# Kernel tuning notes

Measured on AMD Instinct MI355X. Metric: run time of the kernel, lower is better.

Reference implementation:

```python
import jax, jax.numpy as jnp
import numpy as np

D = 1024   # dim == seq_len L (forced by final proj on [L, L])
N = 16     # SSM state size
K = 3      # conv kernel size, padding=1 -> same length


def setup_inputs() -> dict:
    key = jax.random.key(0)
    ks = jax.random.split(key, 8)
    s = lambda k, shape, sc: (jax.random.normal(k, shape, jnp.float32) * sc)
    return {
        "x": s(ks[0], (2, D, D), 1.0),
        "W_proj": s(ks[1], (D, D), D ** -0.5),
        "b_proj": jnp.zeros((D,), jnp.float32),
        "conv_w": s(ks[2], (D, D, K), (D * K) ** -0.5),  # [out_ch, in_ch, K]
        "conv_b": jnp.zeros((D,), jnp.float32),
        "A_log": jnp.log(jnp.tile(jnp.arange(1, N + 1, dtype=jnp.float32)[None, :], (D, 1))),  # [D, N]
        "W_delta": s(ks[3], (D, D), D ** -0.5),
        "W_B": s(ks[4], (D, N), D ** -0.5),
        "W_C": s(ks[5], (D, N), D ** -0.5),
    }


def _ssm(x, A_log, W_delta, W_B, W_C):
    # Mamba S6 diagonal selective scan. x: [L, D]
    delta = jax.nn.softplus(x @ W_delta)            # [L, D]
    B = x @ W_B                                      # [L, N]
    C = x @ W_C                                      # [L, N]
    A = -jnp.exp(A_log)                              # [D, N]
    Abar = jnp.exp(delta[:, :, None] * A[None])      # [L, D, N]
    Bx = (delta * x)[:, :, None] * B[:, None, :]     # [L, D, N]

    def combine(e1, e2):
        a1, b1 = e1
        a2, b2 = e2
        return a1 * a2, a2 * b1 + b2

    _, h = jax.lax.associative_scan(combine, (Abar, Bx), axis=0)  # h: [L, D, N]
    return jnp.einsum('ldn,ln->ld', h, C)            # [L, D]


def reference(x, W_proj, b_proj, conv_w, conv_b, A_log, W_delta, W_B, W_C):
    p = x @ W_proj.T + b_proj                        # shared proj; [2, L, D]
    xm, xg = p[0], p[1]                              # mirrors `x, x_ = self.proj(x)` unpacking batch==2
    xg = jax.nn.silu(xg)                             # [L, D]
    # Conv1d treats xm as (channels=L, length=D), padding=1 -> same length
    xc = jax.lax.conv_general_dilated(
        xm[None], conv_w, window_strides=(1,), padding=[(1, 1)],
        dimension_numbers=('NCW', 'OIW', 'NCW'))[0] + conv_b[:, None]  # [L, D]
    xc = jax.nn.silu(xc)
    y = _ssm(xc, A_log, W_delta, W_B, W_C)           # [L, D]
    y = y @ xg.T                                     # [L, L]  (x @ x_.transpose(-1,-2))
    return y @ W_proj.T + b_proj                     # final shared proj; [L, L]
```

## Files before the change

kernel.cpp:

```cpp
#include <hip/hip_runtime.h>
#include <math.h>


#define LL 1024
#define DD 1024
#define NS 16
#define CCH 16
#define CLEN 64

typedef short     bf16x8_t __attribute__((ext_vector_type(8)));
typedef float     f32x4_t  __attribute__((ext_vector_type(4)));
typedef unsigned short u16x4_t __attribute__((ext_vector_type(4)));
typedef unsigned short u16x8_t __attribute__((ext_vector_type(8)));

__device__ __forceinline__ float silu_f(float x) { return x / (1.f + expf(-x)); }
__device__ __forceinline__ float softplus_f(float x) {
  return fmaxf(x, 0.f) + log1pf(expf(-fabsf(x)));
}
__device__ __forceinline__ unsigned short f2bf(float f) {
  unsigned int u = __float_as_uint(f);
  u += 0x7fffu + ((u >> 16) & 1u);
  return (unsigned short)(u >> 16);
}

template<int N> __device__ __forceinline__ void s_wait_vmcnt() {
  asm volatile("s_waitcnt vmcnt(%0)" :: "n"(N) : "memory");
}
__device__ __forceinline__ void raw_barrier() {
  asm volatile("s_barrier" ::: "memory");
}

__global__ __launch_bounds__(256) void cast_all(
    const float* __restrict__ x, const float* __restrict__ wp,
    const float* __restrict__ cw, unsigned short* __restrict__ x16,
    unsigned short* __restrict__ wp16, unsigned short* __restrict__ cw16) {
  const size_t i = ((size_t)blockIdx.x * 256 + threadIdx.x) * 4;
  const float* in; unsigned short* out; size_t off;
  if (i < 2097152)      { in = x;  out = x16;  off = 0; }
  else if (i < 3145728) { in = wp; out = wp16; off = 2097152; }
  else                  { in = cw; out = cw16; off = 3145728; }
  const float4 v = *(const float4*)(in + (i - off));
  u16x4_t o; o[0] = f2bf(v.x); o[1] = f2bf(v.y); o[2] = f2bf(v.z); o[3] = f2bf(v.w);
  *(u16x4_t*)(out + (i - off)) = o;
}

__global__ __launch_bounds__(256) void tcastk(const float* __restrict__ W,
                                              unsigned short* __restrict__ out) {
  __shared__ float T[64][65];
  const int t = threadIdx.x;
  const int r = t >> 2, cq = (t & 3) << 4;
  const int d0 = blockIdx.x * 64, k0 = blockIdx.y * 64;
  #pragma unroll
  for (int c = 0; c < 16; c += 4) {
    float4 v = *(const float4*)&W[(size_t)(k0 + r) * DD + d0 + cq + c];
    T[r][cq + c + 0] = v.x; T[r][cq + c + 1] = v.y;
    T[r][cq + c + 2] = v.z; T[r][cq + c + 3] = v.w;
  }
  __syncthreads();
  u16x8_t o0, o1;
  #pragma unroll
  for (int j = 0; j < 8; ++j) o0[j] = f2bf(T[cq + j][r]);
  #pragma unroll
  for (int j = 0; j < 8; ++j) o1[j] = f2bf(T[cq + 8 + j][r]);
  *(u16x8_t*)&out[(size_t)(d0 + r) * DD + k0 + cq] = o0;
  *(u16x8_t*)&out[(size_t)(d0 + r) * DD + k0 + cq + 8] = o1;
}

__global__ __launch_bounds__(256) void bct_cast(const float* __restrict__ WB,
                                                const float* __restrict__ WC,
                                                unsigned short* __restrict__ wcomb) {
  const int b = blockIdx.x;
  const int k = threadIdx.x * 4;
  u16x4_t o;
  if (b < 32) {
    const float* W = (b < 16) ? WB : WC;
    const int n = b & 15;
    #pragma unroll
    for (int j = 0; j < 4; ++j) o[j] = f2bf(W[(size_t)(k + j) * NS + n]);
  } else {
    o[0] = o[1] = o[2] = o[3] = 0;
  }
  *(u16x4_t*)&wcomb[(size_t)(1024 + b) * DD + k] = o;
}

__global__ __launch_bounds__(256) void build_xsht(const unsigned short* __restrict__ xm,
                                                  unsigned short* __restrict__ out) {
  __shared__ unsigned short Xs[64][66];
  const int t = threadIdx.x;
  const int w0 = blockIdx.x * 64, i0 = blockIdx.y * 64;
  {
    const int r = t >> 2, cq = (t & 3) << 4;
    #pragma unroll
    for (int c = 0; c < 16; c += 4) {
      u16x4_t v = *(const u16x4_t*)&xm[(size_t)(i0 + r) * DD + w0 + cq + c];
      Xs[r][1 + cq + c + 0] = v[0]; Xs[r][1 + cq + c + 1] = v[1];
      Xs[r][1 + cq + c + 2] = v[2]; Xs[r][1 + cq + c + 3] = v[3];
    }
  }
  if (t < 64)                 Xs[t][0]       = (w0 > 0)        ? xm[(size_t)(i0 + t) * DD + w0 - 1]  : (unsigned short)0;
  else if (t < 128) { int r = t - 64; Xs[r][65] = (w0 + 64 < DD) ? xm[(size_t)(i0 + r) * DD + w0 + 64] : (unsigned short)0; }
  __syncthreads();
  const int wr = t >> 2, q = t & 3;
  unsigned short vals[48];
  #pragma unroll
  for (int ii = 0; ii < 16; ++ii)
    #pragma unroll
    for (int k = 0; k < 3; ++k)
      vals[ii * 3 + k] = Xs[q * 16 + ii][wr + k];
  #pragma unroll
  for (int s = 0; s < 6; ++s) {
    u16x8_t o;
    #pragma unroll
    for (int j = 0; j < 8; ++j) o[j] = vals[s * 8 + j];
    *(u16x8_t*)&out[(size_t)(w0 + wr) * 3072 + (size_t)i0 * 3 + q * 48 + s * 8] = o;
  }
}

template<int ACT, bool BROW, bool O32, bool O16, bool PART>
__global__ __launch_bounds__(256) void gemm_bf16(
    const unsigned short* __restrict__ A, const unsigned short* __restrict__ B,
    const float* __restrict__ bias, float* __restrict__ C32,
    unsigned short* __restrict__ C16, int M, int N, int K, int Ksl,
    size_t sliceStride)
{
  constexpr int GI = 4;
  __shared__ unsigned short s[3][128 * 64];
  const int tid  = threadIdx.x;
  const int lane = tid & 63;
  const int wv   = tid >> 6;
  const int wm   = wv >> 1, wn = wv & 1;
  const int m0 = blockIdx.y * 64, n0 = blockIdx.x * 64;
  const int wbase = tid & 192;
  const int koff = PART ? blockIdx.z * Ksl : 0;

  f32x4_t acc[2][2];
  #pragma unroll
  for (int i = 0; i < 2; ++i)
    #pragma unroll
    for (int j = 0; j < 2; ++j)
      acc[i][j] = (f32x4_t)(0.f);

  auto stage = [&](int buf, int kbase) {
    #pragma unroll
    for (int it = 0; it < GI; ++it) {
      const int c   = (it << 8) + tid;
      const int r   = c >> 3;
      const int kcg = (c & 7) ^ (r & 7);
      const unsigned short* src = (r < 64)
          ? (A + (size_t)(m0 + r) * K + kbase + kcg * 8)
          : (B + (size_t)(n0 + r - 64) * K + kbase + kcg * 8);
      __builtin_amdgcn_global_load_lds(
          (const __attribute__((address_space(1))) void*)src,
          (__attribute__((address_space(3))) void*)(&s[buf][0] + (size_t)((it << 8) + wbase) * 8),
          16, 0, 0);
    }
  };

  const int NT = Ksl >> 6;
  stage(0, koff);
  stage(1, koff + 64);
  s_wait_vmcnt<GI>();
  raw_barrier();

  for (int t = 0; t < NT; ++t) {
    if (t + 2 < NT) stage((t + 2) % 3, koff + (t + 2) * 64);

    const unsigned short* sb = &s[t % 3][0];
    const int rl = lane & 15, kq = lane >> 4;
    bf16x8_t af[2][2], bfr[2][2];
    #pragma unroll
    for (int mi = 0; mi < 2; ++mi) {
      const int row = wm * 32 + mi * 16 + rl;
      #pragma unroll
      for (int ks = 0; ks < 2; ++ks) {
        const int ch = row * 8 + ((ks * 4 + kq) ^ (row & 7));
        af[mi][ks] = *(const bf16x8_t*)(sb + (size_t)ch * 8);
      }
    }
    #pragma unroll
    for (int ni = 0; ni < 2; ++ni) {
      const int row = 64 + wn * 32 + ni * 16 + rl;
      #pragma unroll
      for (int ks = 0; ks < 2; ++ks) {
        const int ch = row * 8 + ((ks * 4 + kq) ^ (row & 7));
        bfr[ni][ks] = *(const bf16x8_t*)(sb + (size_t)ch * 8);
      }
    }
    #pragma unroll
    for (int mi = 0; mi < 2; ++mi)
      #pragma unroll
      for (int ni = 0; ni < 2; ++ni)
        #pragma unroll
        for (int ks = 0; ks < 2; ++ks)
          acc[mi][ni] = __builtin_amdgcn_mfma_f32_16x16x32_bf16(
              af[mi][ks], bfr[ni][ks], acc[mi][ni], 0, 0, 0);

    if (t + 1 < NT) {
      if (t + 2 < NT) s_wait_vmcnt<GI>();
      else            s_wait_vmcnt<0>();
      raw_barrier();
    }
  }

  const int rl = lane & 15, rg = lane >> 4;
  float* outp = PART ? (C32 + (size_t)blockIdx.z * sliceStride) : C32;
  #pragma unroll
  for (int mi = 0; mi < 2; ++mi) {
    #pragma unroll
    for (int ni = 0; ni < 2; ++ni) {
      const int col = n0 + wn * 32 + ni * 16 + rl;
      #pragma unroll
      for (int j = 0; j < 4; ++j) {
        const int row = m0 + wm * 32 + mi * 16 + rg * 4 + j;
        float v = acc[mi][ni][j];
        if (PART) {
          outp[(size_t)row * N + col] = v;
        } else {
          if (bias) v += BROW ? bias[row] : bias[col];
          if (ACT == 1) v = silu_f(v);
          else if (ACT == 2) v = softplus_f(v);
          else if (ACT == 3) { if (row >= 1024) v = silu_f(v); }
          else if (ACT == 4) { if (row < 1024)  v = softplus_f(v); }
          if (O32) C32[(size_t)row * N + col] = v;
          if (O16) C16[(size_t)row * N + col] = f2bf(v);
        }
      }
    }
  }
}

template<int SK, int ACT, bool O32, bool O16>
__global__ __launch_bounds__(256) void reduce_k(
    const float* __restrict__ part, size_t sliceStride,
    const float* __restrict__ bias,
    float* __restrict__ C32, unsigned short* __restrict__ C16)
{
  const size_t idx = ((size_t)blockIdx.x * 256 + threadIdx.x) * 4;
  const int row = (int)(idx >> 10), col = (int)(idx & 1023);
  float4 s = *(const float4*)&part[idx];
  #pragma unroll
  for (int z = 1; z < SK; ++z) {
    const float4 p = *(const float4*)&part[(size_t)z * sliceStride + idx];
    s.x += p.x; s.y += p.y; s.z += p.z; s.w += p.w;
  }
  float v[4] = {s.x, s.y, s.z, s.w};
  if (bias) {
    const float4 bv = *(const float4*)&bias[col];
    v[0] += bv.x; v[1] += bv.y; v[2] += bv.z; v[3] += bv.w;
  }
  #pragma unroll
  for (int j = 0; j < 4; ++j) {
    if (ACT == 2) v[j] = softplus_f(v[j]);
    else if (ACT == 4) { if (row < 1024) v[j] = softplus_f(v[j]); }
  }
  if (O32) { float4 o; o.x = v[0]; o.y = v[1]; o.z = v[2]; o.w = v[3];
             *(float4*)&C32[idx] = o; }
  if (O16) { u16x4_t o; o[0] = f2bf(v[0]); o[1] = f2bf(v[1]);
             o[2] = f2bf(v[2]); o[3] = f2bf(v[3]);
             *(u16x4_t*)&C16[idx] = o; }
}

template<int SK>
__global__ __launch_bounds__(256) void reduce_conv_t(
    const float* __restrict__ part, const float* __restrict__ cb,
    unsigned short* __restrict__ xc16, float* __restrict__ xcT)
{
  __shared__ float T[64][65];
  const int t = threadIdx.x;
  const int r = t >> 4;
  const int cq = (t & 15) << 2;
  const int r0 = blockIdx.y * 64, c0 = blockIdx.x * 64;
  #pragma unroll
  for (int rr = 0; rr < 64; rr += 16) {
    const int row = r0 + r + rr;
    const size_t base = (size_t)row * 1024 + c0 + cq;
    float4 s = *(const float4*)&part[base];
    #pragma unroll
    for (int z = 1; z < SK; ++z) {
      const float4 p = *(const float4*)&part[(size_t)z * (1024 * 1024) + base];
      s.x += p.x; s.y += p.y; s.z += p.z; s.w += p.w;
    }
    const float b = cb[row];
    float v[4] = {silu_f(s.x + b), silu_f(s.y + b), silu_f(s.z + b), silu_f(s.w + b)};
    u16x4_t o16; o16[0] = f2bf(v[0]); o16[1] = f2bf(v[1]);
    o16[2] = f2bf(v[2]); o16[3] = f2bf(v[3]);
    *(u16x4_t*)&xc16[base] = o16;
    T[r + rr][cq + 0] = v[0]; T[r + rr][cq + 1] = v[1];
    T[r + rr][cq + 2] = v[2]; T[r + rr][cq + 3] = v[3];
  }
  __syncthreads();
  #pragma unroll
  for (int rr = 0; rr < 64; rr += 16) {
    float4 o;
    o.x = T[cq + 0][r + rr]; o.y = T[cq + 1][r + rr];
    o.z = T[cq + 2][r + rr]; o.w = T[cq + 3][r + rr];
    *(float4*)&xcT[(size_t)(c0 + r + rr) * LL + r0 + cq] = o;
  }
}

__global__ __launch_bounds__(256) void scan_p1(
    const float* __restrict__ deltaT, const float* __restrict__ xcT,
    const float* __restrict__ BT, const float* __restrict__ A_log,
    float* __restrict__ P, float* __restrict__ H)
{
  const int tid = threadIdx.x;
  const int n = tid & 15, dl = tid >> 4;
  const int d = blockIdx.y * 16 + dl;
  const int c = blockIdx.x;
  const int l0 = c * CLEN;
  const float Av = -expf(A_log[d * NS + n]);
  float h = 0.f, p = 1.f;
  for (int j = 0; j < CLEN; j += 4) {
    const float4 dv = *(const float4*)&deltaT[(size_t)d * LL + l0 + j];
    const float4 xv = *(const float4*)&xcT[(size_t)d * LL + l0 + j];
    const float4 bv = *(const float4*)&BT[(size_t)n * LL + l0 + j];
    const float dvu[4] = {dv.x, dv.y, dv.z, dv.w};
    const float xvu[4] = {xv.x, xv.y, xv.z, xv.w};
    const float bvu[4] = {bv.x, bv.y, bv.z, bv.w};
    #pragma unroll
    for (int u = 0; u < 4; ++u) {
      const float ab = expf(dvu[u] * Av);
      h = fmaf(ab, h, dvu[u] * xvu[u] * bvu[u]);
      p *= ab;
    }
  }
  const int idx = d * NS + n;
  P[(size_t)c * (DD * NS) + idx] = p;
  H[(size_t)c * (DD * NS) + idx] = h;
}

__global__ __launch_bounds__(256) void scan_p2(const float* __restrict__ P,
                                               const float* __restrict__ H,
                                               float* __restrict__ Hin) {
  const int idx = blockIdx.x * 256 + threadIdx.x;
  float hin = 0.f;
  Hin[idx] = 0.f;
  #pragma unroll
  for (int c = 1; c < CCH; ++c) {
    hin = fmaf(P[(size_t)(c - 1) * (DD * NS) + idx], hin,
               H[(size_t)(c - 1) * (DD * NS) + idx]);
    Hin[(size_t)c * (DD * NS) + idx] = hin;
  }
}

__global__ __launch_bounds__(256) void scan_p3(
    const float* __restrict__ deltaT, const float* __restrict__ xcT,
    const float* __restrict__ BT, const float* __restrict__ CT,
    const float* __restrict__ Hin, const float* __restrict__ A_log,
    unsigned short* __restrict__ y16)
{
  const int tid = threadIdx.x;
  const int n = tid & 15, dl = tid >> 4;
  const int d = blockIdx.y * 16 + dl;
  const int c = blockIdx.x;
  const int l0 = c * CLEN;
  const float Av = -expf(A_log[d * NS + n]);
  float h = Hin[(size_t)c * (DD * NS) + d * NS + n];
  for (int j = 0; j < CLEN; j += 4) {
    const float4 dv = *(const float4*)&deltaT[(size_t)d * LL + l0 + j];
    const float4 xv = *(const float4*)&xcT[(size_t)d * LL + l0 + j];
    const float4 bv = *(const float4*)&BT[(size_t)n * LL + l0 + j];
    const float4 cv = *(const float4*)&CT[(size_t)n * LL + l0 + j];
    const float dvu[4] = {dv.x, dv.y, dv.z, dv.w};
    const float xvu[4] = {xv.x, xv.y, xv.z, xv.w};
    const float bvu[4] = {bv.x, bv.y, bv.z, bv.w};
    const float cvu[4] = {cv.x, cv.y, cv.z, cv.w};
    #pragma unroll
    for (int u = 0; u < 4; ++u) {
      const int l = l0 + j + u;
      const float ab = expf(dvu[u] * Av);
      h = fmaf(ab, h, dvu[u] * xvu[u] * bvu[u]);
      float contrib = h * cvu[u];
      contrib += __shfl_xor(contrib, 1);
      contrib += __shfl_xor(contrib, 2);
      contrib += __shfl_xor(contrib, 4);
      contrib += __shfl_xor(contrib, 8);
      if (n == 0) y16[(size_t)l * DD + d] = f2bf(contrib);
    }
  }
}

extern "C" void kernel_launch(void* const* d_in, const int* in_sizes, int n_in,
                              void* d_out, int out_size, void* d_ws, size_t ws_size,
                              hipStream_t stream) {
  const float* x       = (const float*)d_in[0];
  const float* W_proj  = (const float*)d_in[1];
  const float* b_proj  = (const float*)d_in[2];
  const float* conv_w  = (const float*)d_in[3];
  const float* conv_b  = (const float*)d_in[4];
  const float* A_log   = (const float*)d_in[5];
  const float* W_delta = (const float*)d_in[6];
  const float* W_B     = (const float*)d_in[7];
  const float* W_C     = (const float*)d_in[8];
  float* out = (float*)d_out;

  char* w = (char*)d_ws;
  const size_t QMB = 256 * 1024;
  unsigned short* wp16    = (unsigned short*)(w);
  unsigned short* pbuf    = (unsigned short*)(w + 8  * QMB);
  unsigned short* xm16    = pbuf;
  unsigned short* xg16    = pbuf + 1024 * 1024;
  unsigned short* wcomb16 = (unsigned short*)(w + 24 * QMB);
  unsigned short* xc16    = (unsigned short*)(w + 34 * QMB);
  float*          xcT32   = (float*)(w + 42 * QMB);
  unsigned short* x16     = (unsigned short*)(w + 58 * QMB);
  float*          dcomb32 = (float*)(w + 58 * QMB);
  float*          deltaT32= dcomb32;
  float*          BT32    = dcomb32 + (size_t)1024 * 1024;
  float*          CT32    = dcomb32 + (size_t)1040 * 1024;
  unsigned short* cw16    = (unsigned short*)(w + 75 * QMB);
  unsigned short* y16     = (unsigned short*)(w + 75 * QMB);
  float*          Pc      = (float*)(w + 83 * QMB);
  float*          Hc      = (float*)(w + 87 * QMB);
  float*          HinC    = (float*)(w + 91 * QMB);
  unsigned short* out116  = (unsigned short*)(w + 87 * QMB);
  unsigned short* xsht    = (unsigned short*)(w + 99 * QMB);
  float*          part    = (float*)(w + 123 * QMB);
  (void)ws_size;

  const dim3 blk(256);

  cast_all<<<dim3(6144), blk, 0, stream>>>(x, W_proj, conv_w, x16, wp16, cw16);
  tcastk<<<dim3(16, 16), blk, 0, stream>>>(W_delta, wcomb16);
  bct_cast<<<dim3(128), blk, 0, stream>>>(W_B, W_C, wcomb16);

  gemm_bf16<3, false, false, true, false><<<dim3(16, 32), blk, 0, stream>>>(
      x16, wp16, b_proj, nullptr, pbuf, 2048, 1024, 1024, 1024, 0);
  build_xsht<<<dim3(16, 16), blk, 0, stream>>>(xm16, xsht);
  gemm_bf16<0, false, true, false, true><<<dim3(16, 16, 2), blk, 0, stream>>>(
      cw16, xsht, nullptr, part, nullptr, 1024, 1024, 3072, 1536,
      (size_t)1024 * 1024);
  reduce_conv_t<2><<<dim3(16, 16), blk, 0, stream>>>(part, conv_b, xc16, xcT32);
  gemm_bf16<0, false, true, false, true><<<dim3(16, 18, 2), blk, 0, stream>>>(
      wcomb16, xc16, nullptr, part, nullptr, 1152, 1024, 1024, 512,
      (size_t)1152 * 1024);
  reduce_k<2, 4, true, false><<<dim3(1056), blk, 0, stream>>>(
      part, (size_t)1152 * 1024, nullptr, dcomb32, nullptr);
  scan_p1<<<dim3(CCH, DD / 16), blk, 0, stream>>>(deltaT32, xcT32, BT32, A_log, Pc, Hc);
  scan_p2<<<dim3(64), blk, 0, stream>>>(Pc, Hc, HinC);
  scan_p3<<<dim3(CCH, DD / 16), blk, 0, stream>>>(deltaT32, xcT32, BT32, CT32, HinC, A_log, y16);
  gemm_bf16<0, false, true, false, true><<<dim3(16, 16, 2), blk, 0, stream>>>(
      y16, xg16, nullptr, part, nullptr, 1024, 1024, 1024, 512,
      (size_t)1024 * 1024);
  reduce_k<2, 0, false, true><<<dim3(1024), blk, 0, stream>>>(
      part, (size_t)1024 * 1024, nullptr, nullptr, out116);
  gemm_bf16<0, false, true, false, true><<<dim3(16, 16, 2), blk, 0, stream>>>(
      out116, wp16, nullptr, part, nullptr, 1024, 1024, 1024, 512,
      (size_t)1024 * 1024);
  reduce_k<2, 0, true, false><<<dim3(1024), blk, 0, stream>>>(
      part, (size_t)1024 * 1024, b_proj, out, nullptr);
}
```

Measured before the change: 203.3 us.

## Merge prep casts, drop split-K reductions, fold scan carry into final pass

Fuses the three weight and input cast kernels into one launch. Removes split-K from the delta/B/C, y@xg^T and final projection GEMMs, so each writes its epilogue directly and the reduce_k kernels go away. Also trims the padded row count of the combined weight. The scan's separate carry-propagation kernel is removed, and each chunk recomputes its incoming state serially from the per-chunk products. This cuts launches and partial-sum traffic, at the cost of fewer workgroups per GEMM (256 on a large GPU) and redundant carry work in later chunks.

```diff
diff --git a/kernel.cpp b/kernel.cpp
--- a/kernel.cpp
+++ b/kernel.cpp
@@ -30,57 +30,56 @@
   asm volatile("s_barrier" ::: "memory");
 }
 
-__global__ __launch_bounds__(256) void cast_all(
+__global__ __launch_bounds__(256) void prep_all(
     const float* __restrict__ x, const float* __restrict__ wp,
-    const float* __restrict__ cw, unsigned short* __restrict__ x16,
-    unsigned short* __restrict__ wp16, unsigned short* __restrict__ cw16) {
-  const size_t i = ((size_t)blockIdx.x * 256 + threadIdx.x) * 4;
-  const float* in; unsigned short* out; size_t off;
-  if (i < 2097152)      { in = x;  out = x16;  off = 0; }
-  else if (i < 3145728) { in = wp; out = wp16; off = 2097152; }
-  else                  { in = cw; out = cw16; off = 3145728; }
-  const float4 v = *(const float4*)(in + (i - off));
-  u16x4_t o; o[0] = f2bf(v.x); o[1] = f2bf(v.y); o[2] = f2bf(v.z); o[3] = f2bf(v.w);
-  *(u16x4_t*)(out + (i - off)) = o;
-}
-
-__global__ __launch_bounds__(256) void tcastk(const float* __restrict__ W,
-                                              unsigned short* __restrict__ out) {
-  __shared__ float T[64][65];
+    const float* __restrict__ cw, const float* __restrict__ wd,
+    const float* __restrict__ WB, const float* __restrict__ WC,
+    unsigned short* __restrict__ x16, unsigned short* __restrict__ wp16,
+    unsigned short* __restrict__ cw16, unsigned short* __restrict__ wcomb) {
+  const int b = blockIdx.x;
   const int t = threadIdx.x;
-  const int r = t >> 2, cq = (t & 3) << 4;
-  const int d0 = blockIdx.x * 64, k0 = blockIdx.y * 64;
-  #pragma unroll
-  for (int c = 0; c < 16; c += 4) {
-    float4 v = *(const float4*)&W[(size_t)(k0 + r) * DD + d0 + cq + c];
-    T[r][cq + c + 0] = v.x; T[r][cq + c + 1] = v.y;
-    T[r][cq + c + 2] = v.z; T[r][cq + c + 3] = v.w;
-  }
-  __syncthreads();
-  u16x8_t o0, o1;
-  #pragma unroll
-  for (int j = 0; j < 8; ++j) o0[j] = f2bf(T[cq + j][r]);
-  #pragma unroll
-  for (int j = 0; j < 8; ++j) o1[j] = f2bf(T[cq + 8 + j][r]);
-  *(u16x8_t*)&out[(size_t)(d0 + r) * DD + k0 + cq] = o0;
-  *(u16x8_t*)&out[(size_t)(d0 + r) * DD + k0 + cq + 8] = o1;
-}
-
-__global__ __launch_bounds__(256) void bct_cast(const float* __restrict__ WB,
-                                                const float* __restrict__ WC,
-                                                unsigned short* __restrict__ wcomb) {
-  const int b = blockIdx.x;
-  const int k = threadIdx.x * 4;
-  u16x4_t o;
-  if (b < 32) {
-    const float* W = (b < 16) ? WB : WC;
-    const int n = b & 15;
-    #pragma unroll
-    for (int j = 0; j < 4; ++j) o[j] = f2bf(W[(size_t)(k + j) * NS + n]);
+  if (b < 6144) {
+    const size_t i = ((size_t)b * 256 + t) * 4;
+    const float* in; unsigned short* out; size_t off;
+    if (i < 2097152)      { in = x;  out = x16;  off = 0; }
+    else if (i < 3145728) { in = wp; out = wp16; off = 2097152; }
+    else                  { in = cw; out = cw16; off = 3145728; }
+    const float4 v = *(const float4*)(in + (i - off));
+    u16x4_t o; o[0] = f2bf(v.x); o[1] = f2bf(v.y); o[2] = f2bf(v.z); o[3] = f2bf(v.w);
+    *(u16x4_t*)(out + (i - off)) = o;
+  } else if (b < 6400) {
+    __shared__ float T[64][65];
+    const int bi = b - 6144;
+    const int d0 = (bi & 15) << 6, k0 = (bi >> 4) << 6;
+    const int r = t >> 2, cq = (t & 3) << 4;
+    #pragma unroll
+    for (int c = 0; c < 16; c += 4) {
+      float4 v = *(const float4*)&wd[(size_t)(k0 + r) * DD + d0 + cq + c];
+      T[r][cq + c + 0] = v.x; T[r][cq + c + 1] = v.y;
+      T[r][cq + c + 2] = v.z; T[r][cq + c + 3] = v.w;
+    }
+    __syncthreads();
+    u16x8_t o0, o1;
+    #pragma unroll
+    for (int j = 0; j < 8; ++j) o0[j] = f2bf(T[cq + j][r]);
+    #pragma unroll
+    for (int j = 0; j < 8; ++j) o1[j] = f2bf(T[cq + 8 + j][r]);
+    *(u16x8_t*)&wcomb[(size_t)(d0 + r) * DD + k0 + cq] = o0;
+    *(u16x8_t*)&wcomb[(size_t)(d0 + r) * DD + k0 + cq + 8] = o1;
   } else {
-    o[0] = o[1] = o[2] = o[3] = 0;
-  }
-  *(u16x4_t*)&wcomb[(size_t)(1024 + b) * DD + k] = o;
+    const int bb = b - 6400;
+    const int k = t * 4;
+    u16x4_t o;
+    if (bb < 32) {
+      const float* W = (bb < 16) ? WB : WC;
+      const int n = bb & 15;
+      #pragma unroll
+      for (int j = 0; j < 4; ++j) o[j] = f2bf(W[(size_t)(k + j) * NS + n]);
+    } else {
+      o[0] = o[1] = o[2] = o[3] = 0;
+    }
+    *(u16x4_t*)&wcomb[(size_t)(1024 + bb) * DD + k] = o;
+  }
 }
 
 __global__ __launch_bounds__(256) void build_xsht(const unsigned short* __restrict__ xm,
@@ -229,38 +228,6 @@
   }
 }
 
-template<int SK, int ACT, bool O32, bool O16>
-__global__ __launch_bounds__(256) void reduce_k(
-    const float* __restrict__ part, size_t sliceStride,
-    const float* __restrict__ bias,
-    float* __restrict__ C32, unsigned short* __restrict__ C16)
-{
-  const size_t idx = ((size_t)blockIdx.x * 256 + threadIdx.x) * 4;
-  const int row = (int)(idx >> 10), col = (int)(idx & 1023);
-  float4 s = *(const float4*)&part[idx];
-  #pragma unroll
-  for (int z = 1; z < SK; ++z) {
-    const float4 p = *(const float4*)&part[(size_t)z * sliceStride + idx];
-    s.x += p.x; s.y += p.y; s.z += p.z; s.w += p.w;
-  }
-  float v[4] = {s.x, s.y, s.z, s.w};
-  if (bias) {
-    const float4 bv = *(const float4*)&bias[col];
-    v[0] += bv.x; v[1] += bv.y; v[2] += bv.z; v[3] += bv.w;
-  }
-  #pragma unroll
-  for (int j = 0; j < 4; ++j) {
-    if (ACT == 2) v[j] = softplus_f(v[j]);
-    else if (ACT == 4) { if (row < 1024) v[j] = softplus_f(v[j]); }
-  }
-  if (O32) { float4 o; o.x = v[0]; o.y = v[1]; o.z = v[2]; o.w = v[3];
-             *(float4*)&C32[idx] = o; }
-  if (O16) { u16x4_t o; o[0] = f2bf(v[0]); o[1] = f2bf(v[1]);
-             o[2] = f2bf(v[2]); o[3] = f2bf(v[3]);
-             *(u16x4_t*)&C16[idx] = o; }
-}
-
-template<int SK>
 __global__ __launch_bounds__(256) void reduce_conv_t(
     const float* __restrict__ part, const float* __restrict__ cb,
     unsigned short* __restrict__ xc16, float* __restrict__ xcT)
@@ -275,11 +242,8 @@
     const int row = r0 + r + rr;
     const size_t base = (size_t)row * 1024 + c0 + cq;
     float4 s = *(const float4*)&part[base];
-    #pragma unroll
-    for (int z = 1; z < SK; ++z) {
-      const float4 p = *(const float4*)&part[(size_t)z * (1024 * 1024) + base];
-      s.x += p.x; s.y += p.y; s.z += p.z; s.w += p.w;
-    }
+    const float4 p = *(const float4*)&part[(size_t)(1024 * 1024) + base];
+    s.x += p.x; s.y += p.y; s.z += p.z; s.w += p.w;
     const float b = cb[row];
     float v[4] = {silu_f(s.x + b), silu_f(s.y + b), silu_f(s.z + b), silu_f(s.w + b)};
     u16x4_t o16; o16[0] = f2bf(v[0]); o16[1] = f2bf(v[1]);
@@ -329,33 +293,22 @@
   H[(size_t)c * (DD * NS) + idx] = h;
 }
 
-__global__ __launch_bounds__(256) void scan_p2(const float* __restrict__ P,
-                                               const float* __restrict__ H,
-                                               float* __restrict__ Hin) {
-  const int idx = blockIdx.x * 256 + threadIdx.x;
-  float hin = 0.f;
-  Hin[idx] = 0.f;
-  #pragma unroll
-  for (int c = 1; c < CCH; ++c) {
-    hin = fmaf(P[(size_t)(c - 1) * (DD * NS) + idx], hin,
-               H[(size_t)(c - 1) * (DD * NS) + idx]);
-    Hin[(size_t)c * (DD * NS) + idx] = hin;
-  }
-}
-
-__global__ __launch_bounds__(256) void scan_p3(
+__global__ __launch_bounds__(256) void scan_p3c(
     const float* __restrict__ deltaT, const float* __restrict__ xcT,
     const float* __restrict__ BT, const float* __restrict__ CT,
-    const float* __restrict__ Hin, const float* __restrict__ A_log,
-    unsigned short* __restrict__ y16)
+    const float* __restrict__ P, const float* __restrict__ Hc,
+    const float* __restrict__ A_log, unsigned short* __restrict__ y16)
 {
   const int tid = threadIdx.x;
   const int n = tid & 15, dl = tid >> 4;
   const int d = blockIdx.y * 16 + dl;
   const int c = blockIdx.x;
   const int l0 = c * CLEN;
-  const float Av = -expf(A_log[d * NS + n]);
-  float h = Hin[(size_t)c * (DD * NS) + d * NS + n];
+  const int idx = d * NS + n;
+  const float Av = -expf(A_log[idx]);
+  float h = 0.f;
+  for (int cc = 0; cc < c; ++cc)
+    h = fmaf(P[(size_t)cc * (DD * NS) + idx], h, Hc[(size_t)cc * (DD * NS) + idx]);
   for (int j = 0; j < CLEN; j += 4) {
     const float4 dv = *(const float4*)&deltaT[(size_t)d * LL + l0 + j];
     const float4 xv = *(const float4*)&xcT[(size_t)d * LL + l0 + j];
@@ -412,7 +365,6 @@
   unsigned short* y16     = (unsigned short*)(w + 75 * QMB);
   float*          Pc      = (float*)(w + 83 * QMB);
   float*          Hc      = (float*)(w + 87 * QMB);
-  float*          HinC    = (float*)(w + 91 * QMB);
   unsigned short* out116  = (unsigned short*)(w + 87 * QMB);
   unsigned short* xsht    = (unsigned short*)(w + 99 * QMB);
   float*          part    = (float*)(w + 123 * QMB);
@@ -420,33 +372,22 @@
 
   const dim3 blk(256);
 
-  cast_all<<<dim3(6144), blk, 0, stream>>>(x, W_proj, conv_w, x16, wp16, cw16);
-  tcastk<<<dim3(16, 16), blk, 0, stream>>>(W_delta, wcomb16);
-  bct_cast<<<dim3(128), blk, 0, stream>>>(W_B, W_C, wcomb16);
-
+  prep_all<<<dim3(6528), blk, 0, stream>>>(x, W_proj, conv_w, W_delta, W_B, W_C,
+                                           x16, wp16, cw16, wcomb16);
   gemm_bf16<3, false, false, true, false><<<dim3(16, 32), blk, 0, stream>>>(
       x16, wp16, b_proj, nullptr, pbuf, 2048, 1024, 1024, 1024, 0);
   build_xsht<<<dim3(16, 16), blk, 0, stream>>>(xm16, xsht);
   gemm_bf16<0, false, true, false, true><<<dim3(16, 16, 2), blk, 0, stream>>>(
       cw16, xsht, nullptr, part, nullptr, 1024, 1024, 3072, 1536,
       (size_t)1024 * 1024);
-  reduce_conv_t<2><<<dim3(16, 16), blk, 0, stream>>>(part, conv_b, xc16, xcT32);
-  gemm_bf16<0, false, true, false, true><<<dim3(16, 18, 2), blk, 0, stream>>>(
-      wcomb16, xc16, nullptr, part, nullptr, 1152, 1024, 1024, 512,
-      (size_t)1152 * 1024);
-  reduce_k<2, 4, true, false><<<dim3(1056), blk, 0, stream>>>(
-      part, (size_t)1152 * 1024, nullptr, dcomb32, nullptr);
+  reduce_conv_t<<<dim3(16, 16), blk, 0, stream>>>(part, conv_b, xc16, xcT32);
+  gemm_bf16<4, false, true, false, false><<<dim3(16, 17), blk, 0, stream>>>(
+      wcomb16, xc16, nullptr, dcomb32, nullptr, 1088, 1024, 1024, 1024, 0);
   scan_p1<<<dim3(CCH, DD / 16), blk, 0, stream>>>(deltaT32, xcT32, BT32, A_log, Pc, Hc);
-  scan_p2<<<dim3(64), blk, 0, stream>>>(Pc, Hc, HinC);
-  scan_p3<<<dim3(CCH, DD / 16), blk, 0, stream>>>(deltaT32, xcT32, BT32, CT32, HinC, A_log, y16);
-  gemm_bf16<0, false, true, false, true><<<dim3(16, 16, 2), blk, 0, stream>>>(
-      y16, xg16, nullptr, part, nullptr, 1024, 1024, 1024, 512,
-      (size_t)1024 * 1024);
-  reduce_k<2, 0, false, true><<<dim3(1024), blk, 0, stream>>>(
-      part, (size_t)1024 * 1024, nullptr, nullptr, out116);
-  gemm_bf16<0, false, true, false, true><<<dim3(16, 16, 2), blk, 0, stream>>>(
-      out116, wp16, nullptr, part, nullptr, 1024, 1024, 1024, 512,
-      (size_t)1024 * 1024);
-  reduce_k<2, 0, true, false><<<dim3(1024), blk, 0, stream>>>(
-      part, (size_t)1024 * 1024, b_proj, out, nullptr);
-}
+  scan_p3c<<<dim3(CCH, DD / 16), blk, 0, stream>>>(deltaT32, xcT32, BT32, CT32,
+                                                   Pc, Hc, A_log, y16);
+  gemm_bf16<0, false, false, true, false><<<dim3(16, 16), blk, 0, stream>>>(
+      y16, xg16, nullptr, nullptr, out116, 1024, 1024, 1024, 1024, 0);
+  gemm_bf16<0, false, true, false, false><<<dim3(16, 16), blk, 0, stream>>>(
+      out116, wp16, b_proj, out, nullptr, 1024, 1024, 1024, 1024, 0);
+}
```

Result: faster. 192.9 us (-5.1%).
